# Optimization experiments

Hardware: AMD Instinct MI355X
Metric: run time of the kernel (lower is better)

The kernel has to match this reference:

```python
import jax, jax.numpy as jnp
import numpy as np
from jax import lax

B, T_ENC, T_DEC, D, MEL, PRE = 64, 300, 500, 512, 80, 256
K, C_LOC = 31, 32


def setup_inputs() -> dict:
    key = jax.random.key(0)
    ks = iter(jax.random.split(key, 40))
    def w(shape, s=0.05):
        return jax.random.normal(next(ks), shape, dtype=jnp.float32) * s
    zb = lambda n: jnp.zeros((n,), jnp.float32)
    return {
        "enc": w((B, T_ENC, D), 1.0),
        "mel_in": w((B, T_DEC, MEL), 1.0),
        "prenet_w1": w((PRE, MEL)), "prenet_b1": zb(PRE),
        "prenet_w2": w((PRE, PRE)), "prenet_b2": zb(PRE),
        "att_wih": w((4 * D, D + PRE)), "att_whh": w((4 * D, D)),
        "att_bih": zb(4 * D), "att_bhh": zb(4 * D),
        "dec_wih": w((4 * D, 2 * D)), "dec_whh": w((4 * D, D)),
        "dec_bih": zb(4 * D), "dec_bhh": zb(4 * D),
        "q_w": w((D, D)), "q_b": zb(D),
        "mem_w": w((D, D)), "mem_b": zb(D),
        "loc_conv_w": w((C_LOC, 2, K)), "loc_conv_b": zb(C_LOC),
        "loc_proj_w": w((D, C_LOC)), "loc_proj_b": zb(D),
        "v_w": w((1, D)), "v_b": zb(1),
        "mel_w": w((MEL, D)), "mel_b": zb(MEL),
        "stop_w": w((1, D)), "stop_b": zb(1),
    }


def _lstm(x, h, c, wih, whh, bih, bhh):
    # torch.nn.LSTMCell math: gates = x W_ih^T + b_ih + h W_hh^T + b_hh
    g = x @ wih.T + bih + h @ whh.T + bhh
    i, f, gg, o = jnp.split(g, 4, axis=-1)
    c = jax.nn.sigmoid(f) * c + jax.nn.sigmoid(i) * jnp.tanh(gg)
    h = jax.nn.sigmoid(o) * jnp.tanh(c)
    return h, c


def reference(enc, mel_in, prenet_w1, prenet_b1, prenet_w2, prenet_b2,
              att_wih, att_whh, att_bih, att_bhh,
              dec_wih, dec_whh, dec_bih, dec_bhh,
              q_w, q_b, mem_w, mem_b,
              loc_conv_w, loc_conv_b, loc_proj_w, loc_proj_b,
              v_w, v_b, mel_w, mel_b, stop_w, stop_b):
    # Eval mode (dropout/zoneout off), teacher_forcing=1.0 -> prev_mel = mel_in[:, t].
    Bb, T_enc, Dd = enc.shape
    pad = (loc_conv_w.shape[-1] - 1) // 2
    mproj = enc @ mem_w.T + mem_b  # [B, T_enc, D] (hoisted; constant across steps)

    def step(carry, prev_mel):
        ctx, a, a_cum, h_att, c_att, h_dec, c_dec = carry
        # prenet: two Linear+ReLU (dropout off in eval)
        pm = jax.nn.relu(jax.nn.relu(prev_mel @ prenet_w1.T + prenet_b1) @ prenet_w2.T + prenet_b2)
        h_att, c_att = _lstm(jnp.concatenate([pm, ctx], -1), h_att, c_att,
                             att_wih, att_whh, att_bih, att_bhh)
        # location-sensitive attention
        loc = jnp.stack([a, a_cum], axis=1)  # [B, 2, T_enc]
        conv = lax.conv_general_dilated(loc, loc_conv_w, (1,), [(pad, pad)],
                                        dimension_numbers=("NCH", "OIH", "NCH"))
        conv = conv + loc_conv_b[None, :, None]  # [B, C_loc, T_enc]
        loc_feat = jnp.einsum("bct,dc->btd", conv, loc_proj_w) + loc_proj_b  # [B, T_enc, D]
        q = (h_att @ q_w.T + q_b)[:, None, :]  # [B, 1, D]
        e = jnp.tanh(q + mproj + loc_feat) @ v_w[0] + v_b[0]  # [B, T_enc]
        a = jax.nn.softmax(e, axis=1)
        ctx = jnp.einsum("bt,btd->bd", a, enc)
        a_cum = a_cum + a
        h_dec, c_dec = _lstm(jnp.concatenate([h_att, ctx], -1), h_dec, c_dec,
                             dec_wih, dec_whh, dec_bih, dec_bhh)
        mel = h_dec @ mel_w.T + mel_b          # [B, mel_dim]
        stop = h_dec @ stop_w[0] + stop_b[0]   # [B]
        return (ctx, a, a_cum, h_att, c_att, h_dec, c_dec), (mel, stop)

    z = lambda *s: jnp.zeros(s, enc.dtype)
    init = (z(Bb, Dd), z(Bb, T_enc), z(Bb, T_enc), z(Bb, Dd), z(Bb, Dd), z(Bb, Dd), z(Bb, Dd))
    _, (mels, stops) = lax.scan(step, init, jnp.swapaxes(mel_in, 0, 1))
    mel_out = jnp.swapaxes(mels, 0, 1)    # [B, T_dec, mel_dim]
    stop_out = jnp.swapaxes(stops, 0, 1)  # [B, T_dec]
    return mel_out, stop_out
```

## Files before the change

### kernel.cpp

```cpp
#include <hip/hip_runtime.h>
#include <hip/hip_bf16.h>


#define DEV __device__ __forceinline__
typedef __hip_bfloat16 bf16;
DEV float b2f(bf16 x) { return __bfloat162float(x); }
DEV unsigned short f2us(float f) { bf16 h = __float2bfloat16(f); unsigned short u; __builtin_memcpy(&u, &h, 2); return u; }
DEV float us2f(unsigned short u) { union { float f; unsigned int i; } c; c.i = ((unsigned)u) << 16; return c.f; }

constexpr int NB = 256;

__device__ float g_enc[64*300*512];
__device__ __align__(16) float g_melT[500*80*64];
__device__ __align__(16) float g_w1[256*80];
__device__ float g_b1[256];
__device__ __align__(16) float g_w2[256*256];
__device__ float g_b2[256];
__device__ __align__(16) float g_awih[2048*768];
__device__ __align__(16) float g_awhh[2048*512];
__device__ float g_ab[2048];
__device__ __align__(16) float g_dwih[2048*1024];
__device__ __align__(16) float g_dwhh[2048*512];
__device__ float g_db[2048];
__device__ __align__(16) float g_qwt[512*512];
__device__ float g_qpb[512];
__device__ __align__(16) float g_memwt[512*512];
__device__ float g_memb[512];
__device__ float g_cw[32*62];
__device__ float g_cb[32];
__device__ __align__(16) float g_pw[512*32];
__device__ float g_vw[512];
__device__ __align__(16) float g_melw[80*512];
__device__ float g_melb[80];
__device__ __align__(16) float g_stopw[512];
__device__ float g_scal[2];
__device__ int   g_f32io;
__device__ __align__(16) float g_hatt4[2*512*64];
__device__ __align__(16) float g_hattT[64*512];
__device__ float g_catt[512*64];
__device__ __align__(16) float g_hdec4[2*512*64];
__device__ float g_cdec[512*64];
__device__ __align__(16) float g_ctx4[512*64];
__device__ float g_a[64*300];
__device__ float g_acum[64*300];
__device__ __align__(16) float g_pmt4[256*64];
__device__ __align__(16) float g_pm1t4[256*64];
__device__ float g_e[64*300];
__device__ int g_flag[NB*32];
__device__ int g_go[16*32];

struct InPtrs { const void* p[28]; };

DEV float sigf(float x) { return 1.f / (1.f + __expf(-x)); }
DEV float tanhf_fast(float x) {
  float e = __expf(-2.f * fabsf(x));
  float r = (1.f - e) / (1.f + e);
  return copysignf(r, x);
}
DEV int zero_vgpr() { int z; asm volatile("v_mov_b32 %0, 0" : "=v"(z)); return z; }

DEV float ald(const float* p) {
  return __hip_atomic_load(p, __ATOMIC_RELAXED, __HIP_MEMORY_SCOPE_AGENT);
}
DEV void ast(float* p, float v) {
  __hip_atomic_store(p, v, __ATOMIC_RELAXED, __HIP_MEMORY_SCOPE_AGENT);
}
DEV float2 ald2(const float* p) {
  unsigned long long u = __hip_atomic_load((const unsigned long long*)p,
                                           __ATOMIC_RELAXED, __HIP_MEMORY_SCOPE_AGENT);
  union { unsigned long long u; float2 f; } c; c.u = u; return c.f;
}

DEV int detect_f32(const void* enc_raw) {
  const unsigned short* u = (const unsigned short*)enc_raw;
  int big = 0;
  for (int i = 0; i < 256; i += 2) { int e = (u[i] >> 7) & 0xFF; big += (e > 133) ? 1 : 0; }
  return big >= 8 ? 1 : 0;
}
DEV float ldin(const void* p, int i, int f32) {
  return f32 ? ((const float*)p)[i] : b2f(((const bf16*)p)[i]);
}

__global__ __launch_bounds__(256) void k_convert(InPtrs P) {
  const int NT = gridDim.x * 256;
  const int flat = blockIdx.x * 256 + threadIdx.x;
  const int f32 = detect_f32(P.p[0]);
  if (flat == 0) {
    g_f32io = f32;
    g_scal[0] = ldin(P.p[23], 0, f32);
    g_scal[1] = ldin(P.p[27], 0, f32);
  }
#define CVT(dst, idx, n) for (int i = flat; i < (n); i += NT) dst[i] = ldin(P.p[idx], i, f32);
  CVT(g_enc, 0, 64*300*512)
  CVT(g_w1, 2, 256*80)   CVT(g_b1, 3, 256)
  CVT(g_w2, 4, 256*256)  CVT(g_b2, 5, 256)
  CVT(g_awih, 6, 2048*768)  CVT(g_awhh, 7, 2048*512)
  CVT(g_dwih, 10, 2048*1024) CVT(g_dwhh, 11, 2048*512)
  CVT(g_cw, 18, 32*62) CVT(g_cb, 19, 32)
  CVT(g_pw, 20, 512*32)  CVT(g_vw, 22, 512)
  CVT(g_melw, 24, 80*512) CVT(g_melb, 25, 80)
  CVT(g_stopw, 26, 512)  CVT(g_memb, 17, 512)
#undef CVT
  for (int i = flat; i < 500*80*64; i += NT) {
    int b = i & 63, tm = i >> 6;
    g_melT[i] = ldin(P.p[1], b*40000 + tm, f32);
  }
  for (int i = flat; i < 2048; i += NT) g_ab[i] = ldin(P.p[8], i, f32) + ldin(P.p[9], i, f32);
  for (int i = flat; i < 2048; i += NT) g_db[i] = ldin(P.p[12], i, f32) + ldin(P.p[13], i, f32);
  for (int i = flat; i < 512; i += NT) g_qpb[i] = ldin(P.p[15], i, f32) + ldin(P.p[21], i, f32);
  for (int o = flat; o < 512*512; o += NT) {
    int d = o >> 9, k = o & 511;
    g_memwt[(size_t)k*512 + d] = ldin(P.p[16], o, f32);
    g_qwt[(size_t)k*512 + d]   = ldin(P.p[14], o, f32);
  }
  for (int i = flat; i < 2*512*64; i += NT) { g_hatt4[i] = 0.f; g_hdec4[i] = 0.f; }
  for (int i = flat; i < 512*64; i += NT) { g_catt[i] = 0.f; g_cdec[i] = 0.f; g_ctx4[i] = 0.f; }
  for (int i = flat; i < 64*512; i += NT) g_hattT[i] = 0.f;
  for (int i = flat; i < 64*300; i += NT) { g_a[i] = 0.f; g_acum[i] = 0.f; }
  for (int i = flat; i < NB*32; i += NT) g_flag[i] = 0;
  for (int i = flat; i < 16*32; i += NT) g_go[i] = 0;
}

DEV void gbar(int n, int bb, int tid) {
  asm volatile("s_waitcnt vmcnt(0) lgkmcnt(0)" ::: "memory");
  __syncthreads();
  if (tid == 0)
    __hip_atomic_store(&g_flag[bb*32], n, __ATOMIC_RELAXED, __HIP_MEMORY_SCOPE_AGENT);
  if (bb == 0) {
    if (tid < 256)
      while (__hip_atomic_load(&g_flag[tid*32], __ATOMIC_RELAXED, __HIP_MEMORY_SCOPE_AGENT) < n)
        __builtin_amdgcn_s_sleep(1);
    __syncthreads();
    if (tid < 16)
      __hip_atomic_store(&g_go[tid*32], n, __ATOMIC_RELAXED, __HIP_MEMORY_SCOPE_AGENT);
  } else {
    if (tid == 0) {
      while (__hip_atomic_load(&g_go[(bb>>4)*32], __ATOMIC_RELAXED, __HIP_MEMORY_SCOPE_AGENT) < n)
        __builtin_amdgcn_s_sleep(1);
    }
  }
  __syncthreads();
}

template<int RS>
DEV void pdot16(const float* __restrict__ X4, const float* __restrict__ W0,
                int bbu, int k0, int nk, int lane, float* acc) {
#pragma unroll 2
  for (int k = k0; k < k0 + nk; k += 8) {
    const float* xp = X4 + k*64 + lane*4;
    float2 xa0 = ald2(xp);
    float2 xb0 = ald2(xp + 2);
    float2 xa1 = ald2(xp + 256);
    float2 xb1 = ald2(xp + 258);
#pragma unroll
    for (int g = 0; g < 4; ++g) {
#pragma unroll
      for (int u = 0; u < 4; ++u) {
        const float* wp = W0 + (size_t)(g*512 + bbu*4 + u)*RS + k;
        float4 w0 = *(const float4*)(wp);
        float4 w1 = *(const float4*)(wp + 4);
        float a = acc[g*4+u];
        a = fmaf(w0.x, xa0.x, a); a = fmaf(w0.y, xa0.y, a);
        a = fmaf(w0.z, xb0.x, a); a = fmaf(w0.w, xb0.y, a);
        a = fmaf(w1.x, xa1.x, a); a = fmaf(w1.y, xa1.y, a);
        a = fmaf(w1.z, xb1.x, a); a = fmaf(w1.w, xb1.y, a);
        acc[g*4+u] = a;
      }
    }
  }
}

DEV float dotSg(const float* __restrict__ X4, const float* __restrict__ wr,
                int n, int lane, float acc) {
#pragma unroll 2
  for (int k = 0; k < n; k += 8) {
    const float* xp = X4 + k*64 + lane*4;
    float2 xa0 = ald2(xp);
    float2 xb0 = ald2(xp + 2);
    float2 xa1 = ald2(xp + 256);
    float2 xb1 = ald2(xp + 258);
    float4 u0 = *(const float4*)(wr + k);
    float4 u1 = *(const float4*)(wr + k + 4);
    acc = fmaf(u0.x, xa0.x, acc); acc = fmaf(u0.y, xa0.y, acc);
    acc = fmaf(u0.z, xb0.x, acc); acc = fmaf(u0.w, xb0.y, acc);
    acc = fmaf(u1.x, xa1.x, acc); acc = fmaf(u1.y, xa1.y, acc);
    acc = fmaf(u1.z, xb1.x, acc); acc = fmaf(u1.w, xb1.y, acc);
  }
  return acc;
}

__global__ __launch_bounds__(512) void k_dec(void* outv) {
  const int bb = blockIdx.x;
  const int tid = threadIdx.x;
  const int lane = tid & 63, wv = tid >> 6;
  const int h = wv >> 2, dwv = wv & 3;
  const int f32io = g_f32io;
  const int zi = zero_vgpr();
  bf16* outh = (bf16*)outv;
  float* outf = (float*)outv;

  __shared__ __align__(16) float sbuf[8192];
  __shared__ float part[8][40];
  __shared__ float s_h[512];
  __shared__ float s_aa[664];
  __shared__ float s_cw[2016];

  const int eb = bb >> 2, tt0 = (bb & 3) * 75;
  const int da = dwv*128 + lane*2;
  const int r0 = h*38, nr = 38 - h;
  int bn = 0;

  for (int i = tid; i < 1984; i += 512) s_cw[i] = g_cw[i];
  for (int i = tid; i < 32; i += 512) s_cw[1984 + i] = g_cb[i];
  for (int i = tid; i < 664; i += 512) s_aa[i] = 0.f;
  __syncthreads();

  const int bbu = (bb < 128) ? bb : (bb - 128);
  const int jrow = bbu*4 + dwv;
  float bi, bfg, bgg, bog;
  if (bb < 128) { bi = g_ab[jrow]; bfg = g_ab[512+jrow]; bgg = g_ab[1024+jrow]; bog = g_ab[1536+jrow]; }
  else          { bi = g_db[jrow]; bfg = g_db[512+jrow]; bgg = g_db[1024+jrow]; bog = g_db[1536+jrow]; }
  float prb = 0.f;
  if (bb >= 128 && bb < 148) prb = g_melb[(bb-128)*4 + dwv];
  else if (bb >= 64 && bb < 128) prb = g_b2[(bb-64)*4 + dwv];
  else if (bb >= 192) prb = g_b1[(bb-192)*4 + dwv];

  if (bb >= 192 && tid < 256) {
    float acc = prb;
    const float* mt = g_melT + lane;
    const float* wr = g_w1 + zi + (size_t)((bb-192)*4 + dwv)*80;
#pragma unroll
    for (int m4 = 0; m4 < 20; ++m4) {
      float4 w = *(const float4*)(wr + m4*4);
      acc = fmaf(w.x, mt[(m4*4+0)*64], acc);
      acc = fmaf(w.y, mt[(m4*4+1)*64], acc);
      acc = fmaf(w.z, mt[(m4*4+2)*64], acc);
      acc = fmaf(w.w, mt[(m4*4+3)*64], acc);
    }
    ast(&g_pm1t4[(bb-192)*256 + lane*4 + dwv], fmaxf(acc, 0.f));
  }
  gbar(++bn, bb, tid);

  unsigned int mpq[38];
  {
    float a1[38], a2[38];
#pragma unroll
    for (int r = 0; r < 38; ++r) { a1[r] = 0.f; a2[r] = 0.f; }
    for (int kt = 0; kt < 16; ++kt) {
      __syncthreads();
      for (int i = tid; i < 75*32; i += 512) {
        int r = i >> 5, kk = i & 31;
        sbuf[i] = g_enc[((size_t)eb*300 + tt0 + r)*512 + kt*32 + kk];
      }
      __syncthreads();
      for (int kk = 0; kk < 32; ++kk) {
        const int k = kt*32 + kk;
        const float2 w = *(const float2*)(g_memwt + (size_t)k*512 + da);
#pragma unroll
        for (int r = 0; r < 38; ++r) {
          const float ev = sbuf[(r0 + r)*32 + kk];
          a1[r] = fmaf(ev, w.x, a1[r]);
          a2[r] = fmaf(ev, w.y, a2[r]);
        }
      }
    }
    const float2 mb = *(const float2*)(g_memb + da);
#pragma unroll
    for (int r = 0; r < 38; ++r)
      mpq[r] = (unsigned)f2us(a1[r] + mb.x) | ((unsigned)f2us(a2[r] + mb.y) << 16);
    if (bb >= 64 && bb < 128 && wv < 4) {
      float acc = dotSg(g_pm1t4, g_w2 + zi + (size_t)((bb-64)*4 + dwv)*256, 256, lane, prb);
      ast(&g_pmt4[(bb-64)*256 + lane*4 + dwv], fmaxf(acc, 0.f));
    }
  }
  float Pa[32], Pb[32];
#pragma unroll
  for (int i = 0; i < 8; ++i) {
    float4 u = *(const float4*)(g_pw + (size_t)da*32 + 4*i);
    float4 w = *(const float4*)(g_pw + (size_t)(da+1)*32 + 4*i);
    Pa[4*i] = u.x; Pa[4*i+1] = u.y; Pa[4*i+2] = u.z; Pa[4*i+3] = u.w;
    Pb[4*i] = w.x; Pb[4*i+1] = w.y; Pb[4*i+2] = w.z; Pb[4*i+3] = w.w;
  }
  const float2 vv  = *(const float2*)(g_vw + da);
  const float2 qb2 = *(const float2*)(g_qpb + da);
  const float v1 = vv.x, v2 = vv.y;
  const float vb = g_scal[0];
  gbar(++bn, bb, tid);

  for (int t = 0; t <= 500; ++t) {
    const int rp = t & 1, wp = rp ^ 1;

    if (bb < 128) {
      if (t < 500) {
        float acc[16];
#pragma unroll
        for (int r = 0; r < 16; ++r) acc[r] = 0.f;
        pdot16<768>(g_pmt4, g_awih + zi, bb, wv*32, 32, lane, acc);
        pdot16<768>(g_ctx4, g_awih + zi + 256, bb, wv*64, 64, lane, acc);
        pdot16<512>(g_hatt4 + rp*(512*64), g_awhh + zi, bb, wv*64, 64, lane, acc);
#pragma unroll
        for (int r = 0; r < 16; ++r) sbuf[r*512 + wv*64 + lane] = acc[r];
        __syncthreads();
        if (wv < 4) {
          float s0 = bi, s1 = bfg, s2 = bgg, s3 = bog;
#pragma unroll
          for (int w = 0; w < 8; ++w) {
            s0 += sbuf[(dwv)*512      + w*64 + lane];
            s1 += sbuf[(4 + dwv)*512  + w*64 + lane];
            s2 += sbuf[(8 + dwv)*512  + w*64 + lane];
            s3 += sbuf[(12 + dwv)*512 + w*64 + lane];
          }
          const float c = g_catt[jrow*64 + lane];
          const float cn = sigf(s1)*c + sigf(s0)*tanhf_fast(s2);
          const float hn = sigf(s3)*tanhf_fast(cn);
          g_catt[jrow*64 + lane] = cn;
          ast(&g_hatt4[wp*(512*64) + bb*256 + lane*4 + dwv], hn);
          ast(&g_hattT[lane*512 + jrow], hn);
        }
      }
    } else {
      if (t > 0) {
        float acc[16];
#pragma unroll
        for (int r = 0; r < 16; ++r) acc[r] = 0.f;
        pdot16<1024>(g_hatt4 + rp*(512*64), g_dwih + zi, bbu, wv*64, 64, lane, acc);
        pdot16<1024>(g_ctx4, g_dwih + zi + 512, bbu, wv*64, 64, lane, acc);
        pdot16<512>(g_hdec4 + wp*(512*64), g_dwhh + zi, bbu, wv*64, 64, lane, acc);
#pragma unroll
        for (int r = 0; r < 16; ++r) sbuf[r*512 + wv*64 + lane] = acc[r];
        __syncthreads();
        if (wv < 4) {
          float s0 = bi, s1 = bfg, s2 = bgg, s3 = bog;
#pragma unroll
          for (int w = 0; w < 8; ++w) {
            s0 += sbuf[(dwv)*512      + w*64 + lane];
            s1 += sbuf[(4 + dwv)*512  + w*64 + lane];
            s2 += sbuf[(8 + dwv)*512  + w*64 + lane];
            s3 += sbuf[(12 + dwv)*512 + w*64 + lane];
          }
          const float c = g_cdec[jrow*64 + lane];
          const float cn = sigf(s1)*c + sigf(s0)*tanhf_fast(s2);
          const float hn = sigf(s3)*tanhf_fast(cn);
          g_cdec[jrow*64 + lane] = cn;
          ast(&g_hdec4[rp*(512*64) + (bb-128)*256 + lane*4 + dwv], hn);
        }
      }
    }
    gbar(++bn, bb, tid);

    if (t < 500) {
      s_h[tid] = ald(&g_hattT[eb*512 + tid]);
      if (tid < 300) {
        s_aa[15 + tid]  = ald(&g_a[eb*300 + tid]);
        s_aa[347 + tid] = ald(&g_acum[eb*300 + tid]);
      }
      __syncthreads();
      for (int i = tid; i < 75*32; i += 512) {
        const int ttl = i >> 5, c2 = i & 31;
        const int tt = tt0 + ttl;
        float s = s_cw[1984 + c2];
#pragma unroll
        for (int k = 0; k < 31; ++k) {
          s = fmaf(s_cw[c2*62 + k],      s_aa[tt + k], s);
          s = fmaf(s_cw[c2*62 + 31 + k], s_aa[332 + tt + k], s);
        }
        sbuf[i] = s;
      }
      float q1p = h ? 0.f : qb2.x, q2p = h ? 0.f : qb2.y;
      {
        const int kb = h*256;
#pragma unroll 8
        for (int k = kb; k < kb + 256; k += 2) {
          const float h0 = s_h[k], h1 = s_h[k+1];
          const float2 wA = *(const float2*)(g_qwt + (size_t)k*512 + da);
          const float2 wB = *(const float2*)(g_qwt + (size_t)(k+1)*512 + da);
          q1p = fmaf(wA.x, h0, q1p); q2p = fmaf(wA.y, h0, q2p);
          q1p = fmaf(wB.x, h1, q1p); q2p = fmaf(wB.y, h1, q2p);
        }
      }
      float2* qp = (float2*)(sbuf + 4096);
      qp[wv*64 + lane] = make_float2(q1p, q2p);
      __syncthreads();
      const float2 qA = qp[dwv*64 + lane];
      const float2 qB = qp[(4 + dwv)*64 + lane];
      const float q1 = qA.x + qB.x, q2 = qA.y + qB.y;
#pragma unroll
      for (int i = 0; i < 38; ++i) {
        if (i < nr) {
          const int gi = r0 + i;
          float s1 = q1 + us2f((unsigned short)(mpq[i] & 0xffffu));
          float s2 = q2 + us2f((unsigned short)(mpq[i] >> 16));
          const float4* cr = (const float4*)(sbuf + gi*32);
#pragma unroll
          for (int c4 = 0; c4 < 8; ++c4) {
            const float4 cv = cr[c4];
            s1 = fmaf(Pa[c4*4+0], cv.x, s1); s2 = fmaf(Pb[c4*4+0], cv.x, s2);
            s1 = fmaf(Pa[c4*4+1], cv.y, s1); s2 = fmaf(Pb[c4*4+1], cv.y, s2);
            s1 = fmaf(Pa[c4*4+2], cv.z, s1); s2 = fmaf(Pb[c4*4+2], cv.z, s2);
            s1 = fmaf(Pa[c4*4+3], cv.w, s1); s2 = fmaf(Pb[c4*4+3], cv.w, s2);
          }
          float p = v1*tanhf_fast(s1) + v2*tanhf_fast(s2);
#pragma unroll
          for (int m = 32; m >= 1; m >>= 1) p += __shfl_xor(p, m, 64);
          if (lane == 0) part[wv][i] = p;
        }
      }
      __syncthreads();
      if (tid < 75) {
        float e;
        if (tid < 38) e = part[0][tid] + part[1][tid] + part[2][tid] + part[3][tid];
        else          e = part[4][tid-38] + part[5][tid-38] + part[6][tid-38] + part[7][tid-38];
        ast(&g_e[eb*300 + tt0 + tid], e + vb);
      }
    }
    if (t <= 498 && bb >= 192 && tid < 256) {
      float acc = prb;
      const float* mt = g_melT + (size_t)(t+1)*5120 + lane;
      const float* wr = g_w1 + zi + (size_t)((bb-192)*4 + dwv)*80;
#pragma unroll
      for (int m4 = 0; m4 < 20; ++m4) {
        float4 w = *(const float4*)(wr + m4*4);
        acc = fmaf(w.x, mt[(m4*4+0)*64], acc);
        acc = fmaf(w.y, mt[(m4*4+1)*64], acc);
        acc = fmaf(w.z, mt[(m4*4+2)*64], acc);
        acc = fmaf(w.w, mt[(m4*4+3)*64], acc);
      }
      ast(&g_pm1t4[(bb-192)*256 + lane*4 + dwv], fmaxf(acc, 0.f));
    }
    gbar(++bn, bb, tid);

    if (t < 500) {
      if (bb < 64) {
        float* pl = sbuf; float* red = sbuf + 304;
        const int b_ = bb;
        const float* Ep = g_e + b_*300;
        const float e1 = (tid < 300) ? ald(Ep + tid) : -3e38f;
        red[tid] = e1; __syncthreads();
        for (int s = 256; s > 0; s >>= 1) { if (tid < s) red[tid] = fmaxf(red[tid], red[tid+s]); __syncthreads(); }
        const float mx = red[0]; __syncthreads();
        const float p1 = (tid < 300) ? __expf(e1 - mx) : 0.f;
        if (tid < 300) pl[tid] = p1;
        red[tid] = p1; __syncthreads();
        for (int s = 256; s > 0; s >>= 1) { if (tid < s) red[tid] += red[tid+s]; __syncthreads(); }
        const float inv = 1.f / red[0];
        if (tid < 300) {
          const float av = p1*inv;
          const float oc = ald(&g_acum[b_*300 + tid]);
          ast(&g_a[b_*300 + tid], av);
          ast(&g_acum[b_*300 + tid], oc + av);
        }
        __syncthreads();
        const float* ep = g_enc + (size_t)(b_*300)*512;
        const int dd = tid;
        float acc = 0.f;
#pragma unroll 8
        for (int tt = 0; tt < 300; ++tt) acc = fmaf(pl[tt], ep[(size_t)tt*512 + dd], acc);
        ast(&g_ctx4[(dd >> 2)*256 + b_*4 + (dd & 3)], acc * inv);
      } else if (bb < 128) {
        if (t <= 498 && wv < 4) {
          float acc = dotSg(g_pm1t4, g_w2 + zi + (size_t)((bb-64)*4 + dwv)*256, 256, lane, prb);
          ast(&g_pmt4[(bb-64)*256 + lane*4 + dwv], fmaxf(acc, 0.f));
        }
      }
    }
    if (t > 0 && bb >= 128 && bb < 148 && wv < 4) {
      float acc = dotSg(g_hdec4 + rp*(512*64),
                        g_melw + zi + (size_t)((bb-128)*4 + dwv)*512, 512, lane, prb);
      const int m = (bb-128)*4 + dwv;
      const size_t oidx = (size_t)(lane*500 + (t-1))*80 + m;
      if (f32io) outf[oidx] = acc; else outh[oidx] = __float2bfloat16(acc);
    } else if (t > 0 && bb == 148 && tid < 64) {
      float acc = dotSg(g_hdec4 + rp*(512*64), g_stopw + zi, 512, tid, g_scal[1]);
      const size_t oidx = 2560000 + tid*500 + (t-1);
      if (f32io) outf[oidx] = acc; else outh[oidx] = __float2bfloat16(acc);
    }
    gbar(++bn, bb, tid);
  }
}

extern "C" void kernel_launch(void* const* d_in, const int* in_sizes, int n_in,
                              void* d_out, int out_size, void* d_ws, size_t ws_size,
                              hipStream_t stream) {
  (void)d_ws; (void)ws_size; (void)in_sizes; (void)out_size;
  InPtrs P;
  for (int i = 0; i < 28 && i < n_in; ++i) P.p[i] = d_in[i];
  k_convert<<<dim3(2048), dim3(256), 0, stream>>>(P);
  k_dec<<<dim3(NB), dim3(512), 0, stream>>>(d_out);
}
```

Baseline: 111.0 ms.

## Double block size to 1024 threads, splitting reductions across more waves

Raises the persistent decoder kernel from 512 to 1024 threads per block. The K dimension of the LSTM gate dot products, the query projection and the attention energy rows are split over 16 waves instead of 8, and the context sum is split into two time halves. Loading of attention weights into shared memory moves ahead of the first barrier so it overlaps the LSTM phase. The aim is to shorten each serial step's critical path by using more lanes per CU, at the cost of more shared-memory partial reductions and register pressure under the 1024-thread launch bound.

```diff
diff --git a/kernel.cpp b/kernel.cpp
--- a/kernel.cpp
+++ b/kernel.cpp
@@ -117,6 +117,7 @@
   for (int i = flat; i < 512*64; i += NT) { g_catt[i] = 0.f; g_cdec[i] = 0.f; g_ctx4[i] = 0.f; }
   for (int i = flat; i < 64*512; i += NT) g_hattT[i] = 0.f;
   for (int i = flat; i < 64*300; i += NT) { g_a[i] = 0.f; g_acum[i] = 0.f; }
+  for (int i = flat; i < 256*64; i += NT) { g_pmt4[i] = 0.f; g_pm1t4[i] = 0.f; }
   for (int i = flat; i < NB*32; i += NT) g_flag[i] = 0;
   for (int i = flat; i < 16*32; i += NT) g_go[i] = 0;
 }
@@ -189,46 +190,46 @@
   return acc;
 }
 
-__global__ __launch_bounds__(512) void k_dec(void* outv) {
+__global__ __launch_bounds__(1024) void k_dec(void* outv) {
   const int bb = blockIdx.x;
   const int tid = threadIdx.x;
   const int lane = tid & 63, wv = tid >> 6;
-  const int h = wv >> 2, dwv = wv & 3;
+  const int dq = wv & 3, kq = wv >> 2;
   const int f32io = g_f32io;
   const int zi = zero_vgpr();
   bf16* outh = (bf16*)outv;
   float* outf = (float*)outv;
 
-  __shared__ __align__(16) float sbuf[8192];
-  __shared__ float part[8][40];
+  __shared__ __align__(16) float sbuf[16384];
+  __shared__ float part[16][20];
   __shared__ float s_h[512];
-  __shared__ float s_aa[664];
+  __shared__ float s_aa[704];
   __shared__ float s_cw[2016];
 
   const int eb = bb >> 2, tt0 = (bb & 3) * 75;
-  const int da = dwv*128 + lane*2;
-  const int r0 = h*38, nr = 38 - h;
+  const int da = dq*128 + lane*2;
+  const int r0 = kq*19, nr = (kq < 3) ? 19 : 18;
   int bn = 0;
 
-  for (int i = tid; i < 1984; i += 512) s_cw[i] = g_cw[i];
-  for (int i = tid; i < 32; i += 512) s_cw[1984 + i] = g_cb[i];
-  for (int i = tid; i < 664; i += 512) s_aa[i] = 0.f;
+  for (int i = tid; i < 1984; i += 1024) s_cw[i] = g_cw[i];
+  for (int i = tid; i < 32; i += 1024) s_cw[1984 + i] = g_cb[i];
+  for (int i = tid; i < 704; i += 1024) s_aa[i] = 0.f;
   __syncthreads();
 
   const int bbu = (bb < 128) ? bb : (bb - 128);
-  const int jrow = bbu*4 + dwv;
+  const int jrow = bbu*4 + dq;
   float bi, bfg, bgg, bog;
   if (bb < 128) { bi = g_ab[jrow]; bfg = g_ab[512+jrow]; bgg = g_ab[1024+jrow]; bog = g_ab[1536+jrow]; }
   else          { bi = g_db[jrow]; bfg = g_db[512+jrow]; bgg = g_db[1024+jrow]; bog = g_db[1536+jrow]; }
   float prb = 0.f;
-  if (bb >= 128 && bb < 148) prb = g_melb[(bb-128)*4 + dwv];
-  else if (bb >= 64 && bb < 128) prb = g_b2[(bb-64)*4 + dwv];
-  else if (bb >= 192) prb = g_b1[(bb-192)*4 + dwv];
+  if (bb >= 128 && bb < 148) prb = g_melb[(bb-128)*4 + dq];
+  else if (bb >= 64 && bb < 128) prb = g_b2[(bb-64)*4 + dq];
+  else if (bb >= 192) prb = g_b1[(bb-192)*4 + dq];
 
   if (bb >= 192 && tid < 256) {
     float acc = prb;
     const float* mt = g_melT + lane;
-    const float* wr = g_w1 + zi + (size_t)((bb-192)*4 + dwv)*80;
+    const float* wr = g_w1 + zi + (size_t)((bb-192)*4 + dq)*80;
 #pragma unroll
     for (int m4 = 0; m4 < 20; ++m4) {
       float4 w = *(const float4*)(wr + m4*4);
@@ -237,18 +238,18 @@
       acc = fmaf(w.z, mt[(m4*4+2)*64], acc);
       acc = fmaf(w.w, mt[(m4*4+3)*64], acc);
     }
-    ast(&g_pm1t4[(bb-192)*256 + lane*4 + dwv], fmaxf(acc, 0.f));
+    ast(&g_pm1t4[(bb-192)*256 + lane*4 + dq], fmaxf(acc, 0.f));
   }
   gbar(++bn, bb, tid);
 
-  unsigned int mpq[38];
+  unsigned int mpq[19];
   {
-    float a1[38], a2[38];
-#pragma unroll
-    for (int r = 0; r < 38; ++r) { a1[r] = 0.f; a2[r] = 0.f; }
+    float a1[19], a2[19];
+#pragma unroll
+    for (int r = 0; r < 19; ++r) { a1[r] = 0.f; a2[r] = 0.f; }
     for (int kt = 0; kt < 16; ++kt) {
       __syncthreads();
-      for (int i = tid; i < 75*32; i += 512) {
+      for (int i = tid; i < 75*32; i += 1024) {
         int r = i >> 5, kk = i & 31;
         sbuf[i] = g_enc[((size_t)eb*300 + tt0 + r)*512 + kt*32 + kk];
       }
@@ -257,7 +258,7 @@
         const int k = kt*32 + kk;
         const float2 w = *(const float2*)(g_memwt + (size_t)k*512 + da);
 #pragma unroll
-        for (int r = 0; r < 38; ++r) {
+        for (int r = 0; r < 19; ++r) {
           const float ev = sbuf[(r0 + r)*32 + kk];
           a1[r] = fmaf(ev, w.x, a1[r]);
           a2[r] = fmaf(ev, w.y, a2[r]);
@@ -266,11 +267,11 @@
     }
     const float2 mb = *(const float2*)(g_memb + da);
 #pragma unroll
-    for (int r = 0; r < 38; ++r)
+    for (int r = 0; r < 19; ++r)
       mpq[r] = (unsigned)f2us(a1[r] + mb.x) | ((unsigned)f2us(a2[r] + mb.y) << 16);
     if (bb >= 64 && bb < 128 && wv < 4) {
-      float acc = dotSg(g_pm1t4, g_w2 + zi + (size_t)((bb-64)*4 + dwv)*256, 256, lane, prb);
-      ast(&g_pmt4[(bb-64)*256 + lane*4 + dwv], fmaxf(acc, 0.f));
+      float acc = dotSg(g_pm1t4, g_w2 + zi + (size_t)((bb-64)*4 + dq)*256, 256, lane, prb);
+      ast(&g_pmt4[(bb-64)*256 + lane*4 + dq], fmaxf(acc, 0.f));
     }
   }
   float Pa[32], Pb[32];
@@ -290,31 +291,35 @@
   for (int t = 0; t <= 500; ++t) {
     const int rp = t & 1, wp = rp ^ 1;
 
+    if (t < 500 && tid < 300) {
+      s_aa[15 + tid]  = ald(&g_a[eb*300 + tid]);
+      s_aa[347 + tid] = ald(&g_acum[eb*300 + tid]);
+    }
     if (bb < 128) {
       if (t < 500) {
         float acc[16];
 #pragma unroll
         for (int r = 0; r < 16; ++r) acc[r] = 0.f;
-        pdot16<768>(g_pmt4, g_awih + zi, bb, wv*32, 32, lane, acc);
-        pdot16<768>(g_ctx4, g_awih + zi + 256, bb, wv*64, 64, lane, acc);
-        pdot16<512>(g_hatt4 + rp*(512*64), g_awhh + zi, bb, wv*64, 64, lane, acc);
-#pragma unroll
-        for (int r = 0; r < 16; ++r) sbuf[r*512 + wv*64 + lane] = acc[r];
+        pdot16<768>(g_pmt4, g_awih + zi,       bb, wv*16, 16, lane, acc);
+        pdot16<768>(g_ctx4, g_awih + zi + 256, bb, wv*32, 32, lane, acc);
+        pdot16<512>(g_hatt4 + rp*(512*64), g_awhh + zi, bb, wv*32, 32, lane, acc);
+#pragma unroll
+        for (int r = 0; r < 16; ++r) sbuf[r*1024 + wv*64 + lane] = acc[r];
         __syncthreads();
         if (wv < 4) {
           float s0 = bi, s1 = bfg, s2 = bgg, s3 = bog;
 #pragma unroll
-          for (int w = 0; w < 8; ++w) {
-            s0 += sbuf[(dwv)*512      + w*64 + lane];
-            s1 += sbuf[(4 + dwv)*512  + w*64 + lane];
-            s2 += sbuf[(8 + dwv)*512  + w*64 + lane];
-            s3 += sbuf[(12 + dwv)*512 + w*64 + lane];
+          for (int w = 0; w < 16; ++w) {
+            s0 += sbuf[(dq)*1024      + w*64 + lane];
+            s1 += sbuf[(4 + dq)*1024  + w*64 + lane];
+            s2 += sbuf[(8 + dq)*1024  + w*64 + lane];
+            s3 += sbuf[(12 + dq)*1024 + w*64 + lane];
           }
           const float c = g_catt[jrow*64 + lane];
           const float cn = sigf(s1)*c + sigf(s0)*tanhf_fast(s2);
           const float hn = sigf(s3)*tanhf_fast(cn);
           g_catt[jrow*64 + lane] = cn;
-          ast(&g_hatt4[wp*(512*64) + bb*256 + lane*4 + dwv], hn);
+          ast(&g_hatt4[wp*(512*64) + bb*256 + lane*4 + dq], hn);
           ast(&g_hattT[lane*512 + jrow], hn);
         }
       }
@@ -323,39 +328,35 @@
         float acc[16];
 #pragma unroll
         for (int r = 0; r < 16; ++r) acc[r] = 0.f;
-        pdot16<1024>(g_hatt4 + rp*(512*64), g_dwih + zi, bbu, wv*64, 64, lane, acc);
-        pdot16<1024>(g_ctx4, g_dwih + zi + 512, bbu, wv*64, 64, lane, acc);
-        pdot16<512>(g_hdec4 + wp*(512*64), g_dwhh + zi, bbu, wv*64, 64, lane, acc);
-#pragma unroll
-        for (int r = 0; r < 16; ++r) sbuf[r*512 + wv*64 + lane] = acc[r];
+        pdot16<1024>(g_hatt4 + rp*(512*64), g_dwih + zi,      bbu, wv*32, 32, lane, acc);
+        pdot16<1024>(g_ctx4,               g_dwih + zi + 512, bbu, wv*32, 32, lane, acc);
+        pdot16<512>(g_hdec4 + wp*(512*64), g_dwhh + zi,       bbu, wv*32, 32, lane, acc);
+#pragma unroll
+        for (int r = 0; r < 16; ++r) sbuf[r*1024 + wv*64 + lane] = acc[r];
         __syncthreads();
         if (wv < 4) {
           float s0 = bi, s1 = bfg, s2 = bgg, s3 = bog;
 #pragma unroll
-          for (int w = 0; w < 8; ++w) {
-            s0 += sbuf[(dwv)*512      + w*64 + lane];
-            s1 += sbuf[(4 + dwv)*512  + w*64 + lane];
-            s2 += sbuf[(8 + dwv)*512  + w*64 + lane];
-            s3 += sbuf[(12 + dwv)*512 + w*64 + lane];
+          for (int w = 0; w < 16; ++w) {
+            s0 += sbuf[(dq)*1024      + w*64 + lane];
+            s1 += sbuf[(4 + dq)*1024  + w*64 + lane];
+            s2 += sbuf[(8 + dq)*1024  + w*64 + lane];
+            s3 += sbuf[(12 + dq)*1024 + w*64 + lane];
           }
           const float c = g_cdec[jrow*64 + lane];
           const float cn = sigf(s1)*c + sigf(s0)*tanhf_fast(s2);
           const float hn = sigf(s3)*tanhf_fast(cn);
           g_cdec[jrow*64 + lane] = cn;
-          ast(&g_hdec4[rp*(512*64) + (bb-128)*256 + lane*4 + dwv], hn);
+          ast(&g_hdec4[rp*(512*64) + (bb-128)*256 + lane*4 + dq], hn);
         }
       }
     }
     gbar(++bn, bb, tid);
 
     if (t < 500) {
-      s_h[tid] = ald(&g_hattT[eb*512 + tid]);
-      if (tid < 300) {
-        s_aa[15 + tid]  = ald(&g_a[eb*300 + tid]);
-        s_aa[347 + tid] = ald(&g_acum[eb*300 + tid]);
-      }
+      if (tid < 512) s_h[tid] = ald(&g_hattT[eb*512 + tid]);
       __syncthreads();
-      for (int i = tid; i < 75*32; i += 512) {
+      for (int i = tid; i < 75*32; i += 1024) {
         const int ttl = i >> 5, c2 = i & 31;
         const int tt = tt0 + ttl;
         float s = s_cw[1984 + c2];
@@ -366,26 +367,29 @@
         }
         sbuf[i] = s;
       }
-      float q1p = h ? 0.f : qb2.x, q2p = h ? 0.f : qb2.y;
+      float q1p = (kq == 0) ? qb2.x : 0.f, q2p = (kq == 0) ? qb2.y : 0.f;
       {
-        const int kb = h*256;
+        const int kb = kq*128;
 #pragma unroll 8
-        for (int k = kb; k < kb + 256; k += 2) {
-          const float h0 = s_h[k], h1 = s_h[k+1];
+        for (int k = kb; k < kb + 128; k += 2) {
+          const float2 hh = *(const float2*)(s_h + k);
           const float2 wA = *(const float2*)(g_qwt + (size_t)k*512 + da);
           const float2 wB = *(const float2*)(g_qwt + (size_t)(k+1)*512 + da);
-          q1p = fmaf(wA.x, h0, q1p); q2p = fmaf(wA.y, h0, q2p);
-          q1p = fmaf(wB.x, h1, q1p); q2p = fmaf(wB.y, h1, q2p);
+          q1p = fmaf(wA.x, hh.x, q1p); q2p = fmaf(wA.y, hh.x, q2p);
+          q1p = fmaf(wB.x, hh.y, q1p); q2p = fmaf(wB.y, hh.y, q2p);
         }
       }
       float2* qp = (float2*)(sbuf + 4096);
       qp[wv*64 + lane] = make_float2(q1p, q2p);
       __syncthreads();
-      const float2 qA = qp[dwv*64 + lane];
-      const float2 qB = qp[(4 + dwv)*64 + lane];
-      const float q1 = qA.x + qB.x, q2 = qA.y + qB.y;
-#pragma unroll
-      for (int i = 0; i < 38; ++i) {
+      float q1 = 0.f, q2 = 0.f;
+#pragma unroll
+      for (int K = 0; K < 4; ++K) {
+        const float2 qv = qp[(K*4 + dq)*64 + lane];
+        q1 += qv.x; q2 += qv.y;
+      }
+#pragma unroll
+      for (int i = 0; i < 19; ++i) {
         if (i < nr) {
           const int gi = r0 + i;
           float s1 = q1 + us2f((unsigned short)(mpq[i] & 0xffffu));
@@ -407,16 +411,15 @@
       }
       __syncthreads();
       if (tid < 75) {
-        float e;
-        if (tid < 38) e = part[0][tid] + part[1][tid] + part[2][tid] + part[3][tid];
-        else          e = part[4][tid-38] + part[5][tid-38] + part[6][tid-38] + part[7][tid-38];
+        const int K = tid / 19, ii = tid - K*19;
+        const float e = part[K*4+0][ii] + part[K*4+1][ii] + part[K*4+2][ii] + part[K*4+3][ii];
         ast(&g_e[eb*300 + tt0 + tid], e + vb);
       }
     }
     if (t <= 498 && bb >= 192 && tid < 256) {
       float acc = prb;
       const float* mt = g_melT + (size_t)(t+1)*5120 + lane;
-      const float* wr = g_w1 + zi + (size_t)((bb-192)*4 + dwv)*80;
+      const float* wr = g_w1 + zi + (size_t)((bb-192)*4 + dq)*80;
 #pragma unroll
       for (int m4 = 0; m4 < 20; ++m4) {
         float4 w = *(const float4*)(wr + m4*4);
@@ -425,23 +428,25 @@
         acc = fmaf(w.z, mt[(m4*4+2)*64], acc);
         acc = fmaf(w.w, mt[(m4*4+3)*64], acc);
       }
-      ast(&g_pm1t4[(bb-192)*256 + lane*4 + dwv], fmaxf(acc, 0.f));
+      ast(&g_pm1t4[(bb-192)*256 + lane*4 + dq], fmaxf(acc, 0.f));
     }
     gbar(++bn, bb, tid);
 
     if (t < 500) {
       if (bb < 64) {
-        float* pl = sbuf; float* red = sbuf + 304;
+        float* pl = sbuf;
+        float* red = sbuf + 1024;
+        float* ctxp = sbuf + 2048;
         const int b_ = bb;
         const float* Ep = g_e + b_*300;
         const float e1 = (tid < 300) ? ald(Ep + tid) : -3e38f;
         red[tid] = e1; __syncthreads();
-        for (int s = 256; s > 0; s >>= 1) { if (tid < s) red[tid] = fmaxf(red[tid], red[tid+s]); __syncthreads(); }
+        for (int s = 512; s > 0; s >>= 1) { if (tid < s) red[tid] = fmaxf(red[tid], red[tid+s]); __syncthreads(); }
         const float mx = red[0]; __syncthreads();
         const float p1 = (tid < 300) ? __expf(e1 - mx) : 0.f;
         if (tid < 300) pl[tid] = p1;
         red[tid] = p1; __syncthreads();
-        for (int s = 256; s > 0; s >>= 1) { if (tid < s) red[tid] += red[tid+s]; __syncthreads(); }
+        for (int s = 512; s > 0; s >>= 1) { if (tid < s) red[tid] += red[tid+s]; __syncthreads(); }
         const float inv = 1.f / red[0];
         if (tid < 300) {
           const float av = p1*inv;
@@ -450,23 +455,27 @@
           ast(&g_acum[b_*300 + tid], oc + av);
         }
         __syncthreads();
-        const float* ep = g_enc + (size_t)(b_*300)*512;
-        const int dd = tid;
+        const int half = tid >> 9, dd = tid & 511;
+        const float* ep = g_enc + (size_t)(b_*300 + half*150)*512 + dd;
+        const float* plh = pl + half*150;
         float acc = 0.f;
-#pragma unroll 8
-        for (int tt = 0; tt < 300; ++tt) acc = fmaf(pl[tt], ep[(size_t)tt*512 + dd], acc);
-        ast(&g_ctx4[(dd >> 2)*256 + b_*4 + (dd & 3)], acc * inv);
+#pragma unroll 10
+        for (int tt = 0; tt < 150; ++tt) acc = fmaf(plh[tt], ep[(size_t)tt*512], acc);
+        ctxp[half*512 + dd] = acc;
+        __syncthreads();
+        if (tid < 512)
+          ast(&g_ctx4[(tid >> 2)*256 + b_*4 + (tid & 3)], (ctxp[tid] + ctxp[512 + tid]) * inv);
       } else if (bb < 128) {
         if (t <= 498 && wv < 4) {
-          float acc = dotSg(g_pm1t4, g_w2 + zi + (size_t)((bb-64)*4 + dwv)*256, 256, lane, prb);
-          ast(&g_pmt4[(bb-64)*256 + lane*4 + dwv], fmaxf(acc, 0.f));
+          float acc = dotSg(g_pm1t4, g_w2 + zi + (size_t)((bb-64)*4 + dq)*256, 256, lane, prb);
+          ast(&g_pmt4[(bb-64)*256 + lane*4 + dq], fmaxf(acc, 0.f));
         }
       }
     }
     if (t > 0 && bb >= 128 && bb < 148 && wv < 4) {
       float acc = dotSg(g_hdec4 + rp*(512*64),
-                        g_melw + zi + (size_t)((bb-128)*4 + dwv)*512, 512, lane, prb);
-      const int m = (bb-128)*4 + dwv;
+                        g_melw + zi + (size_t)((bb-128)*4 + dq)*512, 512, lane, prb);
+      const int m = (bb-128)*4 + dq;
       const size_t oidx = (size_t)(lane*500 + (t-1))*80 + m;
       if (f32io) outf[oidx] = acc; else outh[oidx] = __float2bfloat16(acc);
     } else if (t > 0 && bb == 148 && tid < 64) {
@@ -485,5 +494,5 @@
   InPtrs P;
   for (int i = 0; i < 28 && i < n_in; ++i) P.p[i] = d_in[i];
   k_convert<<<dim3(2048), dim3(256), 0, stream>>>(P);
-  k_dec<<<dim3(NB), dim3(512), 0, stream>>>(d_out);
-}
+  k_dec<<<dim3(NB), dim3(1024), 0, stream>>>(d_out);
+}
```

After: 203.0 ms. +82.9%, slower.
